# Optimization experiments

Measured on AMD Instinct MI355X. Metric: run time of the kernel, lower is better.

The kernel has to match this reference:

```python
import math
import jax, jax.numpy as jnp
import numpy as np

N_LAYERS = 30
RC = 64        # residual_channels
N_MELS = 80
TED = 128      # time_emb_dim
CD = 256       # text_dim
B, T = 8, 8192
EPS = 1e-12    # F.normalize eps


def conv1d(x, w, b, dilation=1, padding=0):
    # x: [B,C,T], w: [O,I,K], b: [O]
    y = jax.lax.conv_general_dilated(
        x, w, window_strides=(1,), padding=[(padding, padding)],
        rhs_dilation=(dilation,), dimension_numbers=("NCH", "OIH", "NCH"))
    return y + b[None, :, None]


def sinusoidal_embedding(t, dim):
    half = dim // 2
    freqs = jnp.exp(jnp.arange(half, dtype=jnp.float32) * (-math.log(10000.0) / (half - 1)))
    ang = t.astype(jnp.float32)[:, None] * freqs[None, :]
    return jnp.concatenate([jnp.sin(ang), jnp.cos(ang)], axis=1)  # [B, dim]


def mish(x):
    return x * jnp.tanh(jax.nn.softplus(x))


def setup_inputs() -> dict:
    key = jax.random.key(0)
    ks = jax.random.split(key, 24)
    s = 0.05
    inp = {
        "x": jax.random.normal(ks[0], (B, 1, N_MELS, T), jnp.float32),
        "t": jax.random.randint(ks[1], (B,), 0, 1000),
        "c_emb": jax.random.normal(ks[2], (B, CD), jnp.float32),
        # input_proj: Conv1d(n_mels, RC, 1)
        "in_w": jax.random.normal(ks[3], (RC, N_MELS, 1), jnp.float32) * s,
        "in_b": jnp.zeros((RC,), jnp.float32),
        # time MLP: Linear(TED, 4*TED), Mish, Linear(4*TED, TED). torch weight [out,in]
        "te_w1": jax.random.normal(ks[4], (4 * TED, TED), jnp.float32) * s,
        "te_b1": jnp.zeros((4 * TED,), jnp.float32),
        "te_w2": jax.random.normal(ks[5], (TED, 4 * TED), jnp.float32) * s,
        "te_b2": jnp.zeros((TED,), jnp.float32),
        # per-layer stacked params
        "dconv_w": jax.random.normal(ks[6], (N_LAYERS, 2 * RC, RC, 3), jnp.float32) * s,
        "dconv_b": jnp.zeros((N_LAYERS, 2 * RC), jnp.float32),
        "tproj_w": jax.random.normal(ks[7], (N_LAYERS, 2 * RC, TED), jnp.float32) * s,
        "tproj_b": jnp.zeros((N_LAYERS, 2 * RC), jnp.float32),
        "cproj_w": jax.random.normal(ks[8], (N_LAYERS, 2 * RC, CD), jnp.float32) * s,
        "cproj_b": jnp.zeros((N_LAYERS, 2 * RC), jnp.float32),
        "rs_w": jax.random.normal(ks[9], (N_LAYERS, 2 * RC, RC, 1), jnp.float32) * s,
        "rs_b": jnp.zeros((N_LAYERS, 2 * RC), jnp.float32),
        "skip_w": jax.random.normal(ks[10], (RC, RC, 1), jnp.float32) * s,
        "skip_b": jnp.zeros((RC,), jnp.float32),
        "out_w": jax.random.normal(ks[11], (N_MELS, RC, 1), jnp.float32) * s,
        "out_b": jnp.zeros((N_MELS,), jnp.float32),
    }
    return inp


def reference(x, t, c_emb, in_w, in_b, te_w1, te_b1, te_w2, te_b2,
              dconv_w, dconv_b, tproj_w, tproj_b, cproj_w, cproj_b,
              rs_w, rs_b, skip_w, skip_b, out_w, out_b):
    h = x[:, 0]                                  # squeeze(1) -> [B, n_mels, T]
    h = conv1d(h, in_w, in_b)                    # [B, RC, T]
    te = sinusoidal_embedding(t, TED)
    te = mish(te @ te_w1.T + te_b1) @ te_w2.T + te_b2   # [B, TED]

    skips = jnp.zeros_like(conv1d(h, rs_w[0], rs_b[0])[:, :RC])  # [B, RC, T]
    skips = jnp.zeros((h.shape[0], RC, h.shape[2]), h.dtype)
    for i in range(N_LAYERS):
        dil = 2 ** (i % 10)
        g = conv1d(h, dconv_w[i], dconv_b[i], dilation=dil, padding=dil)  # [B, 2RC, T]
        tp = (te @ tproj_w[i].T + tproj_b[i])[:, :, None]                 # [B, 2RC, 1]
        tp = tp / jnp.maximum(jnp.abs(tp), EPS)      # F.normalize over size-1 dim
        cp = (c_emb @ cproj_w[i].T + cproj_b[i])[:, :, None]
        cp = cp / jnp.maximum(jnp.abs(cp), EPS)
        g = g + tp + cp
        gate, filt = g[:, :RC], g[:, RC:]            # chunk(2, dim=1)
        out = jnp.tanh(filt) * jax.nn.sigmoid(gate)
        rs = conv1d(out, rs_w[i], rs_b[i])           # [B, 2RC, T]
        res, skip = rs[:, :RC], rs[:, RC:]
        h = h + res * (1.0 / math.sqrt(2.0))
        skips = skips + skip

    y = skips / math.sqrt(N_LAYERS)
    y = jax.nn.relu(conv1d(y, skip_w, skip_b))
    y = conv1d(y, out_w, out_b)                      # [B, n_mels, T]
    return y[:, None]                                # unsqueeze(1)
```

## Files before the change

### kernel.cpp

```cpp
#include <hip/hip_runtime.h>
#include <hip/hip_bf16.h>
#include <math.h>

#define NL 30
#define NM 80
#define Bx 8
#define Tx 8192

typedef short short8 __attribute__((ext_vector_type(8)));
typedef float f32x4 __attribute__((ext_vector_type(4)));
typedef unsigned int u32x2 __attribute__((ext_vector_type(2)));
typedef unsigned int u32x4 __attribute__((ext_vector_type(4)));

__device__ __forceinline__ float bf2f(unsigned short u) {
    union { unsigned int u; float f; } v; v.u = ((unsigned int)u) << 16; return v.f;
}
__device__ __forceinline__ unsigned short f2bf(float f) {
    union { float f; unsigned int u; } v; v.f = f;
    unsigned int r = v.u + 0x7FFFu + ((v.u >> 16) & 1u);
    return (unsigned short)(r >> 16);
}

#if defined(__has_builtin)
#if __has_builtin(__builtin_amdgcn_global_load_lds)
#define HAS_GLL 1
#endif
#endif

__device__ __forceinline__ void gll16(const void* g, void* l) {
#ifdef HAS_GLL
    __builtin_amdgcn_global_load_lds(
        (const __attribute__((address_space(1))) void*)g,
        (__attribute__((address_space(3))) void*)l, 16, 0, 0);
#else
    int lane = threadIdx.x & 63;
    *(u32x4*)((char*)l + lane * 16) = *(const u32x4*)((const char*)g + lane * 16);
#endif
}

__device__ __forceinline__ void stageW(const unsigned short* __restrict__ wc,
                                       const unsigned short* __restrict__ wr,
                                       unsigned char* ldsA, unsigned char* ldsR, int tid) {
    int w = tid >> 6, lane = tid & 63;
    #pragma unroll
    for (int j = 0; j < 6; ++j) {
        int cbase = j * 512 + w * 64;
        gll16(wc + (size_t)(cbase + lane) * 8, ldsA + cbase * 16);
    }
    #pragma unroll
    for (int j = 0; j < 2; ++j) {
        int cbase = j * 512 + w * 64;
        gll16(wr + (size_t)(cbase + lane) * 8, ldsR + cbase * 16);
    }
}

__global__ __launch_bounds__(512) void setup_kernel(
        const float* __restrict__ dconv_w, const float* __restrict__ rs_w,
        const float* __restrict__ skip_w, const float* __restrict__ out_w,
        unsigned short* __restrict__ wc2, unsigned short* __restrict__ wr2,
        unsigned short* __restrict__ skw16, unsigned short* __restrict__ oww16,
        const float* __restrict__ x, const float* __restrict__ in_w,
        const float* __restrict__ in_b, unsigned short* __restrict__ h0) {
    __shared__ __align__(16) unsigned char smem[49152];
    int blk = blockIdx.x;
    int tid = threadIdx.x;
    if (blk < 30) {
        int l = blk;
        unsigned short* st = (unsigned short*)smem;
        const f32x4* src4 = (const f32x4*)(dconv_w + (size_t)l * 24576);
        #pragma unroll
        for (int h = 0; h < 2; ++h) {
            f32x4 v[6];
            #pragma unroll
            for (int it = 0; it < 6; ++it)
                v[it] = src4[(h * 6 + it) * 512 + tid];
            #pragma unroll
            for (int it = 0; it < 6; ++it) {
                int chunk = (h * 6 + it) * 512 + tid;
                #pragma unroll
                for (int e = 0; e < 4; ++e) {
                    int sidx = chunk * 4 + e;
                    int oc = sidx / 192;
                    int r = sidx - oc * 192;
                    int ic = r / 3;
                    int tap = r - ic * 3;
                    int dst = tap * 8192 + oc * 64 + (((ic >> 3) ^ (oc & 7)) << 3) + (ic & 7);
                    st[dst] = f2bf(v[it][e]);
                }
            }
        }
        __syncthreads();
        u32x4* dst4 = (u32x4*)(wc2 + (size_t)l * 24576);
        const u32x4* s4 = (const u32x4*)st;
        #pragma unroll
        for (int it = 0; it < 6; ++it)
            dst4[it * 512 + tid] = s4[it * 512 + tid];
    } else if (blk < 60) {
        int l = blk - 30;
        unsigned short* st = (unsigned short*)smem;
        const f32x4* src4 = (const f32x4*)(rs_w + (size_t)l * 8192);
        f32x4 v[4];
        #pragma unroll
        for (int it = 0; it < 4; ++it)
            v[it] = src4[it * 512 + tid];
        #pragma unroll
        for (int it = 0; it < 4; ++it) {
            int chunk = it * 512 + tid;
            #pragma unroll
            for (int e = 0; e < 4; ++e) {
                int sidx = chunk * 4 + e;
                int row = sidx >> 6;
                int ic = sidx & 63;
                int dst = row * 64 + (((ic >> 3) ^ (row & 7)) << 3) + (ic & 7);
                st[dst] = f2bf(v[it][e]);
            }
        }
        __syncthreads();
        u32x4* dst4 = (u32x4*)(wr2 + (size_t)l * 8192);
        const u32x4* s4 = (const u32x4*)st;
        #pragma unroll
        for (int it = 0; it < 2; ++it)
            dst4[it * 512 + tid] = s4[it * 512 + tid];
    } else if (blk == 60) {
        for (int j = tid; j < 4096; j += 512)
            skw16[j] = f2bf(skip_w[j] * 0.18257418583505536f);
        for (int j = tid; j < 5120; j += 512)
            oww16[j] = f2bf(out_w[j]);
    } else {
        float (*wT)[64] = (float(*)[64])smem;
        for (int i = tid; i < NM * 64; i += 512) {
            int m = i >> 6, c = i & 63;
            wT[m][c] = in_w[c * NM + m];
        }
        __syncthreads();
        int j = blk - 61;
        int b = j >> 5;
        int t = (j & 31) * 256 + (tid >> 1);
        int ch0 = (tid & 1) * 32;
        const float* xp = x + (size_t)b * NM * Tx + t;
        float acc[32];
        #pragma unroll
        for (int c = 0; c < 32; ++c) acc[c] = in_b[ch0 + c];
        #pragma unroll 1
        for (int m0 = 0; m0 < NM; m0 += 8) {
            float xv[8];
            #pragma unroll
            for (int u = 0; u < 8; ++u) xv[u] = xp[(size_t)(m0 + u) * Tx];
            #pragma unroll
            for (int u = 0; u < 8; ++u) {
                #pragma unroll
                for (int c = 0; c < 32; ++c)
                    acc[c] = fmaf(xv[u], wT[m0 + u][ch0 + c], acc[c]);
            }
        }
        unsigned short* hp = h0 + ((size_t)b * Tx + t) * 64 + ch0;
        #pragma unroll
        for (int c = 0; c < 32; c += 2) {
            unsigned int p = (unsigned int)f2bf(acc[c]) | ((unsigned int)f2bf(acc[c + 1]) << 16);
            *(unsigned int*)(hp + c) = p;
        }
    }
}

__global__ __launch_bounds__(512) void gbias_kernel(
        const int* __restrict__ tin,
        const float* __restrict__ w1, const float* __restrict__ b1,
        const float* __restrict__ w2, const float* __restrict__ b2,
        const float* __restrict__ cemb,
        const float* __restrict__ tpw, const float* __restrict__ tpb,
        const float* __restrict__ cpw, const float* __restrict__ cpb,
        const float* __restrict__ dcb,
        float* __restrict__ gbias) {
    __shared__ float emb[128];
    __shared__ float h1s[512];
    __shared__ float red[512];
    __shared__ float ted[128];
    int l = blockIdx.x >> 3;
    int b = blockIdx.x & 7;
    int tid = threadIdx.x, wid = tid >> 6, lane = tid & 63;

    if (tid < 64) {
        float fr = expf(-(float)tid * (logf(10000.f) / 63.f));
        float ang = (float)tin[b] * fr;
        emb[tid] = sinf(ang);
        emb[tid + 64] = cosf(ang);
    }
    __syncthreads();
    {
        float a = b1[tid];
        const f32x4* wr4 = (const f32x4*)(w1 + tid * 128);
        #pragma unroll 8
        for (int k = 0; k < 32; ++k) {
            f32x4 w4 = wr4[k];
            a = fmaf(emb[k * 4], w4[0], a);
            a = fmaf(emb[k * 4 + 1], w4[1], a);
            a = fmaf(emb[k * 4 + 2], w4[2], a);
            a = fmaf(emb[k * 4 + 3], w4[3], a);
        }
        float sp = (a > 15.f) ? a : log1pf(expf(a));
        h1s[tid] = a * tanhf(sp);
    }
    __syncthreads();
    {
        int o = tid & 127, q = tid >> 7;
        float p = 0.f;
        const f32x4* wr4 = (const f32x4*)(w2 + o * 512 + q * 128);
        const float* hq = h1s + q * 128;
        #pragma unroll 8
        for (int k = 0; k < 32; ++k) {
            f32x4 w4 = wr4[k];
            p = fmaf(hq[k * 4], w4[0], p);
            p = fmaf(hq[k * 4 + 1], w4[1], p);
            p = fmaf(hq[k * 4 + 2], w4[2], p);
            p = fmaf(hq[k * 4 + 3], w4[3], p);
        }
        red[tid] = p;
    }
    __syncthreads();
    if (tid < 128)
        ted[tid] = b2[tid] + red[tid] + red[tid + 128] + red[tid + 256] + red[tid + 384];
    __syncthreads();

    float te0 = ted[lane];
    float te1 = ted[64 + lane];
    float ce0 = cemb[b * 256 + lane];
    float ce1 = cemb[b * 256 + 64 + lane];
    float ce2 = cemb[b * 256 + 128 + lane];
    float ce3 = cemb[b * 256 + 192 + lane];
    #pragma unroll 4
    for (int i = 0; i < 16; ++i) {
        int ch = i * 8 + wid;
        const float* wr = tpw + (size_t)(l * 128 + ch) * 128;
        float s = te0 * wr[lane] + te1 * wr[lane + 64];
        const float* wc = cpw + (size_t)(l * 128 + ch) * 256;
        float sc = ce0 * wc[lane] + ce1 * wc[lane + 64] + ce2 * wc[lane + 128] + ce3 * wc[lane + 192];
        #pragma unroll
        for (int off = 32; off >= 1; off >>= 1) {
            s += __shfl_xor(s, off, 64);
            sc += __shfl_xor(sc, off, 64);
        }
        if (lane == 0) {
            float tp = tpb[l * 128 + ch] + s;
            float cp = cpb[l * 128 + ch] + sc;
            float s1 = tp / fmaxf(fabsf(tp), 1e-12f);
            float s2 = cp / fmaxf(fabsf(cp), 1e-12f);
            gbias[(l * 8 + b) * 128 + ch] = dcb[l * 128 + ch] + s1 + s2;
        }
    }
}

__launch_bounds__(512, 4)
__global__ void layer_kernel(const unsigned short* __restrict__ h_in,
                             unsigned short* __restrict__ h_out,
                             float* __restrict__ skips,
                             const unsigned short* __restrict__ wc2,
                             const unsigned short* __restrict__ wr2,
                             const float* __restrict__ gbias,
                             const float* __restrict__ rsb,
                             int dil, int first) {
    __shared__ __align__(16) unsigned char lds[81920];
    unsigned char* ldsA = lds;
    unsigned char* ldsR = lds + 49152;
    unsigned char* ldsO = lds + 65536;

    int tid = threadIdx.x;
    int wid = tid >> 6, lane = tid & 63, lr = lane & 15, lq = lane >> 4;

    stageW(wc2, wr2, ldsA, ldsR, tid);

    int bid = blockIdx.x;
    int wg = (bid & 7) * 64 + (bid >> 3);
    int b = wg >> 6;
    int t0 = ((wg & 63) << 7) + wid * 16;

    const unsigned short* hb = h_in + (size_t)b * Tx * 64;
    short8 bv[3][2];
    #pragma unroll
    for (int tap = 0; tap < 3; ++tap) {
        int toff = (tap - 1) * dil;
        int t = t0 + lr + toff;
        bool v = ((unsigned)t < (unsigned)Tx);
        #pragma unroll
        for (int kc = 0; kc < 2; ++kc) {
            short8 z = {0, 0, 0, 0, 0, 0, 0, 0};
            if (v) z = *(const short8*)(hb + t * 64 + kc * 32 + lq * 8);
            bv[tap][kc] = z;
        }
    }

    f32x4 acc[8];
    #pragma unroll
    for (int mf = 0; mf < 8; ++mf)
        acc[mf] = *(const f32x4*)(gbias + b * 128 + mf * 16 + lq * 4);
    __syncthreads();

    #pragma unroll
    for (int tap = 0; tap < 3; ++tap) {
        #pragma unroll
        for (int kc = 0; kc < 2; ++kc) {
            #pragma unroll
            for (int mf = 0; mf < 8; ++mf) {
                int row = tap * 128 + mf * 16 + lr;
                short8 af = *(const short8*)(ldsA + row * 128 + ((kc * 64 + lq * 16) ^ ((lr & 7) << 4)));
                acc[mf] = __builtin_amdgcn_mfma_f32_16x16x32_bf16(af, bv[tap][kc], acc[mf], 0, 0, 0);
            }
        }
    }

    size_t base = ((size_t)b * Tx + t0 + lr) * 64;
    u32x2 hv[4];
    f32x4 sko[4];
    #pragma unroll
    for (int mf = 0; mf < 4; ++mf) {
        hv[mf] = *(const u32x2*)(h_in + base + mf * 16 + lq * 4);
        if (!first) sko[mf] = *(const f32x4*)(skips + base + mf * 16 + lq * 4);
        else { sko[mf][0] = 0.f; sko[mf][1] = 0.f; sko[mf][2] = 0.f; sko[mf][3] = 0.f; }
    }

    unsigned char* myO = ldsO + wid * 2048;
    #pragma unroll
    for (int mf = 0; mf < 4; ++mf) {
        int p = lr;
        unsigned short ob[4];
        #pragma unroll
        for (int r = 0; r < 4; ++r) {
            float g = acc[mf][r];
            float f = acc[mf + 4][r];
            f = fminf(f, 15.f);
            g = fminf(g, 30.f);
            float ea = __builtin_amdgcn_exp2f(f * 2.8853900817779268f);
            float eb = __builtin_amdgcn_exp2f(g * 1.4426950408889634f);
            float num = (ea - 1.f) * eb;
            float den = (ea + 1.f) * (1.f + eb);
            ob[r] = f2bf(num * __builtin_amdgcn_rcpf(den));
        }
        u32x2 pk;
        pk[0] = (unsigned int)ob[0] | ((unsigned int)ob[1] << 16);
        pk[1] = (unsigned int)ob[2] | ((unsigned int)ob[3] << 16);
        *(u32x2*)(myO + p * 128 + ((mf * 32 + lq * 8) ^ ((p & 7) << 4))) = pk;
    }

    const float rt2 = 1.41421356237309505f;
    f32x4 racc[8];
    #pragma unroll
    for (int mf = 0; mf < 4; ++mf) {
        f32x4 rb = *(const f32x4*)(rsb + mf * 16 + lq * 4);
        unsigned short* hp = (unsigned short*)&hv[mf];
        f32x4 r;
        #pragma unroll
        for (int r_ = 0; r_ < 4; ++r_) r[r_] = fmaf(bf2f(hp[r_]), rt2, rb[r_]);
        racc[mf] = r;
    }
    #pragma unroll
    for (int mf = 0; mf < 4; ++mf)
        racc[mf + 4] = *(const f32x4*)(rsb + 64 + mf * 16 + lq * 4) + sko[mf];

    #pragma unroll
    for (int kc = 0; kc < 2; ++kc) {
        int p = lr;
        short8 ov = *(const short8*)(myO + p * 128 + ((kc * 64 + lq * 16) ^ ((p & 7) << 4)));
        #pragma unroll
        for (int mf = 0; mf < 8; ++mf) {
            int row = mf * 16 + lr;
            short8 af = *(const short8*)(ldsR + row * 128 + ((kc * 64 + lq * 16) ^ ((lr & 7) << 4)));
            racc[mf] = __builtin_amdgcn_mfma_f32_16x16x32_bf16(af, ov, racc[mf], 0, 0, 0);
        }
    }

    const float inv_s2 = 0.70710678118654752f;
    #pragma unroll
    for (int mf = 0; mf < 4; ++mf) {
        unsigned short hnew[4];
        #pragma unroll
        for (int r = 0; r < 4; ++r)
            hnew[r] = f2bf(racc[mf][r] * inv_s2);
        u32x2 hw;
        hw[0] = (unsigned int)hnew[0] | ((unsigned int)hnew[1] << 16);
        hw[1] = (unsigned int)hnew[2] | ((unsigned int)hnew[3] << 16);
        *(u32x2*)(h_out + base + mf * 16 + lq * 4) = hw;
        *(f32x4*)(skips + base + mf * 16 + lq * 4) = racc[mf + 4];
    }
}

__launch_bounds__(512, 2)
__global__ void layer_pair_kernel(const unsigned short* __restrict__ h_in,
                                  unsigned short* __restrict__ h_out,
                                  float* __restrict__ skips,
                                  const unsigned short* __restrict__ wc2a,
                                  const unsigned short* __restrict__ wr2a,
                                  const float* __restrict__ gba,
                                  const float* __restrict__ rsba,
                                  int l1, int dil1, int dil2, int ht16, int first) {
    __shared__ __align__(16) unsigned char lds[114688];
    unsigned char* ldsA = lds;
    unsigned char* ldsR = lds + 49152;
    unsigned char* ldsH = lds + 65536;
    unsigned char* ldsO = lds + 90112;

    int tid = threadIdx.x;
    int w = tid >> 6, lane = tid & 63, lr = lane & 15, lq = lane >> 4;
    int l2 = l1 + 1;
    const float rt2 = 1.41421356237309505f;
    const float inv_s2 = 0.70710678118654752f;

    stageW(wc2a + (size_t)l1 * 24576, wr2a + (size_t)l1 * 8192, ldsA, ldsR, tid);

    int bid = blockIdx.x;
    int wg = (bid & 7) * 64 + (bid >> 3);
    int b = wg >> 6;
    int t0 = (wg & 63) << 7;
    int T = 8 + 2 * ht16;
    int ct = (w >= ht16) ? w : 8 + w;

    const unsigned short* hb = h_in + (size_t)b * Tx * 64;
    const float* gb1 = gba + (size_t)(l1 * 8 + b) * 128;
    const float* rsb1 = rsba + (size_t)l1 * 128;
    __syncthreads();

    for (int k = 0; k < 2; ++k) {
        int tile = k ? 8 + w : w;
        if (k && tile >= T) break;
        int gtb = t0 + (tile - ht16) * 16;
        short8 bv[3][2];
        #pragma unroll
        for (int tap = 0; tap < 3; ++tap) {
            int t = gtb + lr + (tap - 1) * dil1;
            bool v = ((unsigned)t < (unsigned)Tx);
            #pragma unroll
            for (int kc = 0; kc < 2; ++kc) {
                short8 z = {0, 0, 0, 0, 0, 0, 0, 0};
                if (v) z = *(const short8*)(hb + t * 64 + kc * 32 + lq * 8);
                bv[tap][kc] = z;
            }
        }
        f32x4 acc[8];
        #pragma unroll
        for (int mf = 0; mf < 8; ++mf)
            acc[mf] = *(const f32x4*)(gb1 + mf * 16 + lq * 4);
        #pragma unroll
        for (int tap = 0; tap < 3; ++tap) {
            #pragma unroll
            for (int kc = 0; kc < 2; ++kc) {
                #pragma unroll
                for (int mf = 0; mf < 8; ++mf) {
                    int row = tap * 128 + mf * 16 + lr;
                    short8 af = *(const short8*)(ldsA + row * 128 + ((kc * 64 + lq * 16) ^ ((lr & 7) << 4)));
                    acc[mf] = __builtin_amdgcn_mfma_f32_16x16x32_bf16(af, bv[tap][kc], acc[mf], 0, 0, 0);
                }
            }
        }
        unsigned char* myO = ldsO + tile * 2048;
        #pragma unroll
        for (int mf = 0; mf < 4; ++mf) {
            int p = lr;
            unsigned short ob[4];
            #pragma unroll
            for (int r = 0; r < 4; ++r) {
                float g = acc[mf][r];
                float f = acc[mf + 4][r];
                f = fminf(f, 15.f);
                g = fminf(g, 30.f);
                float ea = __builtin_amdgcn_exp2f(f * 2.8853900817779268f);
                float eb = __builtin_amdgcn_exp2f(g * 1.4426950408889634f);
                float num = (ea - 1.f) * eb;
                float den = (ea + 1.f) * (1.f + eb);
                ob[r] = f2bf(num * __builtin_amdgcn_rcpf(den));
            }
            u32x2 pk;
            pk[0] = (unsigned int)ob[0] | ((unsigned int)ob[1] << 16);
            pk[1] = (unsigned int)ob[2] | ((unsigned int)ob[3] << 16);
            *(u32x2*)(myO + p * 128 + ((mf * 32 + lq * 8) ^ ((p & 7) << 4))) = pk;
        }
    }

    f32x4 sk1[4];
    u32x2 hn1[4];
    for (int k = 0; k < 2; ++k) {
        int tile = k ? 8 + w : w;
        if (k && tile >= T) break;
        int gtb = t0 + (tile - ht16) * 16;
        int t = gtb + lr;
        bool tv = ((unsigned)t < (unsigned)Tx);
        u32x2 hv[4];
        #pragma unroll
        for (int mf = 0; mf < 4; ++mf) {
            u32x2 z; z[0] = 0u; z[1] = 0u;
            if (tv) z = *(const u32x2*)(h_in + ((size_t)b * Tx + t) * 64 + mf * 16 + lq * 4);
            hv[mf] = z;
        }
        f32x4 racc[8];
        #pragma unroll
        for (int mf = 0; mf < 4; ++mf) {
            f32x4 rb = *(const f32x4*)(rsb1 + mf * 16 + lq * 4);
            unsigned short* hp = (unsigned short*)&hv[mf];
            f32x4 r;
            #pragma unroll
            for (int r_ = 0; r_ < 4; ++r_) r[r_] = fmaf(bf2f(hp[r_]), rt2, rb[r_]);
            racc[mf] = r;
        }
        #pragma unroll
        for (int mf = 0; mf < 4; ++mf)
            racc[mf + 4] = *(const f32x4*)(rsb1 + 64 + mf * 16 + lq * 4);
        unsigned char* myO = ldsO + tile * 2048;
        #pragma unroll
        for (int kc = 0; kc < 2; ++kc) {
            int p = lr;
            short8 ov = *(const short8*)(myO + p * 128 + ((kc * 64 + lq * 16) ^ ((p & 7) << 4)));
            #pragma unroll
            for (int mf = 0; mf < 8; ++mf) {
                int row = mf * 16 + lr;
                short8 af = *(const short8*)(ldsR + row * 128 + ((kc * 64 + lq * 16) ^ ((lr & 7) << 4)));
                racc[mf] = __builtin_amdgcn_mfma_f32_16x16x32_bf16(af, ov, racc[mf], 0, 0, 0);
            }
        }
        int hrow = tile * 16 + lr;
        #pragma unroll
        for (int mf = 0; mf < 4; ++mf) {
            u32x2 pk; pk[0] = 0u; pk[1] = 0u;
            if (tv) {
                unsigned short hn[4];
                #pragma unroll
                for (int r = 0; r < 4; ++r)
                    hn[r] = f2bf(racc[mf][r] * inv_s2);
                pk[0] = (unsigned int)hn[0] | ((unsigned int)hn[1] << 16);
                pk[1] = (unsigned int)hn[2] | ((unsigned int)hn[3] << 16);
            }
            *(u32x2*)(ldsH + hrow * 128 + ((mf * 32 + lq * 8) ^ ((hrow & 7) << 4))) = pk;
            if (tile == ct) { sk1[mf] = racc[mf + 4]; hn1[mf] = pk; }
        }
    }
    __syncthreads();

    stageW(wc2a + (size_t)l2 * 24576, wr2a + (size_t)l2 * 8192, ldsA, ldsR, tid);
    int gtc = t0 + (ct - ht16) * 16;
    size_t cbase = ((size_t)b * Tx + gtc + lr) * 64;
    f32x4 sko[4];
    #pragma unroll
    for (int mf = 0; mf < 4; ++mf) {
        if (!first) sko[mf] = *(const f32x4*)(skips + cbase + mf * 16 + lq * 4);
        else { sko[mf][0] = 0.f; sko[mf][1] = 0.f; sko[mf][2] = 0.f; sko[mf][3] = 0.f; }
    }
    const float* gb2 = gba + (size_t)(l2 * 8 + b) * 128;
    const float* rsb2 = rsba + (size_t)l2 * 128;
    f32x4 acc2[8];
    #pragma unroll
    for (int mf = 0; mf < 8; ++mf)
        acc2[mf] = *(const f32x4*)(gb2 + mf * 16 + lq * 4);
    __syncthreads();

    int lrow0 = ct * 16 + lr;
    #pragma unroll
    for (int tap = 0; tap < 3; ++tap) {
        int row = lrow0 + (tap - 1) * dil2;
        #pragma unroll
        for (int kc = 0; kc < 2; ++kc) {
            short8 bv2 = *(const short8*)(ldsH + row * 128 + ((kc * 64 + lq * 16) ^ ((row & 7) << 4)));
            #pragma unroll
            for (int mf = 0; mf < 8; ++mf) {
                int wrow = tap * 128 + mf * 16 + lr;
                short8 af = *(const short8*)(ldsA + wrow * 128 + ((kc * 64 + lq * 16) ^ ((lr & 7) << 4)));
                acc2[mf] = __builtin_amdgcn_mfma_f32_16x16x32_bf16(af, bv2, acc2[mf], 0, 0, 0);
            }
        }
    }

    unsigned char* myO = ldsO + ct * 2048;
    #pragma unroll
    for (int mf = 0; mf < 4; ++mf) {
        int p = lr;
        unsigned short ob[4];
        #pragma unroll
        for (int r = 0; r < 4; ++r) {
            float g = acc2[mf][r];
            float f = acc2[mf + 4][r];
            f = fminf(f, 15.f);
            g = fminf(g, 30.f);
            float ea = __builtin_amdgcn_exp2f(f * 2.8853900817779268f);
            float eb = __builtin_amdgcn_exp2f(g * 1.4426950408889634f);
            float num = (ea - 1.f) * eb;
            float den = (ea + 1.f) * (1.f + eb);
            ob[r] = f2bf(num * __builtin_amdgcn_rcpf(den));
        }
        u32x2 pk;
        pk[0] = (unsigned int)ob[0] | ((unsigned int)ob[1] << 16);
        pk[1] = (unsigned int)ob[2] | ((unsigned int)ob[3] << 16);
        *(u32x2*)(myO + p * 128 + ((mf * 32 + lq * 8) ^ ((p & 7) << 4))) = pk;
    }

    f32x4 racc2[8];
    #pragma unroll
    for (int mf = 0; mf < 4; ++mf) {
        f32x4 rb = *(const f32x4*)(rsb2 + mf * 16 + lq * 4);
        unsigned short* hp = (unsigned short*)&hn1[mf];
        f32x4 r;
        #pragma unroll
        for (int r_ = 0; r_ < 4; ++r_) r[r_] = fmaf(bf2f(hp[r_]), rt2, rb[r_]);
        racc2[mf] = r;
    }
    #pragma unroll
    for (int mf = 0; mf < 4; ++mf)
        racc2[mf + 4] = *(const f32x4*)(rsb2 + 64 + mf * 16 + lq * 4) + sko[mf] + sk1[mf];

    #pragma unroll
    for (int kc = 0; kc < 2; ++kc) {
        int p = lr;
        short8 ov = *(const short8*)(myO + p * 128 + ((kc * 64 + lq * 16) ^ ((p & 7) << 4)));
        #pragma unroll
        for (int mf = 0; mf < 8; ++mf) {
            int row = mf * 16 + lr;
            short8 af = *(const short8*)(ldsR + row * 128 + ((kc * 64 + lq * 16) ^ ((lr & 7) << 4)));
            racc2[mf] = __builtin_amdgcn_mfma_f32_16x16x32_bf16(af, ov, racc2[mf], 0, 0, 0);
        }
    }

    #pragma unroll
    for (int mf = 0; mf < 4; ++mf) {
        unsigned short hnew[4];
        #pragma unroll
        for (int r = 0; r < 4; ++r)
            hnew[r] = f2bf(racc2[mf][r] * inv_s2);
        u32x2 hw;
        hw[0] = (unsigned int)hnew[0] | ((unsigned int)hnew[1] << 16);
        hw[1] = (unsigned int)hnew[2] | ((unsigned int)hnew[3] << 16);
        *(u32x2*)(h_out + cbase + mf * 16 + lq * 4) = hw;
        *(f32x4*)(skips + cbase + mf * 16 + lq * 4) = racc2[mf + 4];
    }
}

__launch_bounds__(512, 2)
__global__ void layer_last_kernel(const unsigned short* __restrict__ h_in,
                                  const float* __restrict__ skips,
                                  const unsigned short* __restrict__ wc2,
                                  const unsigned short* __restrict__ wr2,
                                  const float* __restrict__ gbias,
                                  const float* __restrict__ rsb,
                                  const unsigned short* __restrict__ skw,
                                  const float* __restrict__ skb,
                                  const unsigned short* __restrict__ oww,
                                  const float* __restrict__ obias,
                                  float* __restrict__ y,
                                  int dil) {
    __shared__ __align__(16) unsigned char lds[81920];
    unsigned char* ldsA = lds;
    unsigned char* ldsR = lds + 49152;
    unsigned char* ldsO = lds + 65536;

    int tid = threadIdx.x;
    int wid = tid >> 6, lane = tid & 63, lr = lane & 15, lq = lane >> 4;

    stageW(wc2, wr2, ldsA, ldsR, tid);

    int bid = blockIdx.x;
    int wg = (bid & 7) * 64 + (bid >> 3);
    int b = wg >> 6;
    int t0 = ((wg & 63) << 7) + wid * 16;

    const unsigned short* hb = h_in + (size_t)b * Tx * 64;
    short8 bv[3][2];
    #pragma unroll
    for (int tap = 0; tap < 3; ++tap) {
        int toff = (tap - 1) * dil;
        int t = t0 + lr + toff;
        bool v = ((unsigned)t < (unsigned)Tx);
        #pragma unroll
        for (int kc = 0; kc < 2; ++kc) {
            short8 z = {0, 0, 0, 0, 0, 0, 0, 0};
            if (v) z = *(const short8*)(hb + t * 64 + kc * 32 + lq * 8);
            bv[tap][kc] = z;
        }
    }

    f32x4 acc[8];
    #pragma unroll
    for (int mf = 0; mf < 8; ++mf)
        acc[mf] = *(const f32x4*)(gbias + b * 128 + mf * 16 + lq * 4);
    __syncthreads();

    #pragma unroll
    for (int tap = 0; tap < 3; ++tap) {
        #pragma unroll
        for (int kc = 0; kc < 2; ++kc) {
            #pragma unroll
            for (int mf = 0; mf < 8; ++mf) {
                int row = tap * 128 + mf * 16 + lr;
                short8 af = *(const short8*)(ldsA + row * 128 + ((kc * 64 + lq * 16) ^ ((lr & 7) << 4)));
                acc[mf] = __builtin_amdgcn_mfma_f32_16x16x32_bf16(af, bv[tap][kc], acc[mf], 0, 0, 0);
            }
        }
    }

    size_t base = ((size_t)b * Tx + t0 + lr) * 64;
    f32x4 sko[4];
    #pragma unroll
    for (int mf = 0; mf < 4; ++mf)
        sko[mf] = *(const f32x4*)(skips + base + mf * 16 + lq * 4);

    unsigned char* myO = ldsO + wid * 2048;
    #pragma unroll
    for (int mf = 0; mf < 4; ++mf) {
        int p = lr;
        unsigned short ob[4];
        #pragma unroll
        for (int r = 0; r < 4; ++r) {
            float g = acc[mf][r];
            float f = acc[mf + 4][r];
            f = fminf(f, 15.f);
            g = fminf(g, 30.f);
            float ea = __builtin_amdgcn_exp2f(f * 2.8853900817779268f);
            float eb = __builtin_amdgcn_exp2f(g * 1.4426950408889634f);
            float num = (ea - 1.f) * eb;
            float den = (ea + 1.f) * (1.f + eb);
            ob[r] = f2bf(num * __builtin_amdgcn_rcpf(den));
        }
        u32x2 pk;
        pk[0] = (unsigned int)ob[0] | ((unsigned int)ob[1] << 16);
        pk[1] = (unsigned int)ob[2] | ((unsigned int)ob[3] << 16);
        *(u32x2*)(myO + p * 128 + ((mf * 32 + lq * 8) ^ ((p & 7) << 4))) = pk;
    }

    f32x4 racc[4];
    #pragma unroll
    for (int mf = 0; mf < 4; ++mf)
        racc[mf] = *(const f32x4*)(rsb + 64 + mf * 16 + lq * 4) + sko[mf];
    #pragma unroll
    for (int kc = 0; kc < 2; ++kc) {
        int p = lr;
        short8 ov = *(const short8*)(myO + p * 128 + ((kc * 64 + lq * 16) ^ ((p & 7) << 4)));
        #pragma unroll
        for (int mf = 0; mf < 4; ++mf) {
            int row = 64 + mf * 16 + lr;
            short8 af = *(const short8*)(ldsR + row * 128 + ((kc * 64 + lq * 16) ^ ((lr & 7) << 4)));
            racc[mf] = __builtin_amdgcn_mfma_f32_16x16x32_bf16(af, ov, racc[mf], 0, 0, 0);
        }
    }

    #pragma unroll
    for (int mf = 0; mf < 4; ++mf) {
        int p = lr;
        u32x2 pk;
        pk[0] = (unsigned int)f2bf(racc[mf][0]) | ((unsigned int)f2bf(racc[mf][1]) << 16);
        pk[1] = (unsigned int)f2bf(racc[mf][2]) | ((unsigned int)f2bf(racc[mf][3]) << 16);
        *(u32x2*)(myO + p * 128 + ((mf * 32 + lq * 8) ^ ((p & 7) << 4))) = pk;
    }

    f32x4 yacc[4];
    #pragma unroll
    for (int mf = 0; mf < 4; ++mf)
        yacc[mf] = *(const f32x4*)(skb + mf * 16 + lq * 4);
    #pragma unroll
    for (int kc = 0; kc < 2; ++kc) {
        int p = lr;
        short8 Bv = *(const short8*)(myO + p * 128 + ((kc * 64 + lq * 16) ^ ((p & 7) << 4)));
        #pragma unroll
        for (int mf = 0; mf < 4; ++mf) {
            short8 A1 = *(const short8*)(skw + (mf * 16 + lr) * 64 + kc * 32 + lq * 8);
            yacc[mf] = __builtin_amdgcn_mfma_f32_16x16x32_bf16(A1, Bv, yacc[mf], 0, 0, 0);
        }
    }
    #pragma unroll
    for (int mf = 0; mf < 4; ++mf) {
        int p = lr;
        u32x2 pk;
        pk[0] = (unsigned int)f2bf(fmaxf(yacc[mf][0], 0.f)) | ((unsigned int)f2bf(fmaxf(yacc[mf][1], 0.f)) << 16);
        pk[1] = (unsigned int)f2bf(fmaxf(yacc[mf][2], 0.f)) | ((unsigned int)f2bf(fmaxf(yacc[mf][3], 0.f)) << 16);
        *(u32x2*)(myO + p * 128 + ((mf * 32 + lq * 8) ^ ((p & 7) << 4))) = pk;
    }

    f32x4 oacc[5];
    #pragma unroll
    for (int mf = 0; mf < 5; ++mf)
        oacc[mf] = *(const f32x4*)(obias + mf * 16 + lq * 4);
    #pragma unroll
    for (int kc = 0; kc < 2; ++kc) {
        int p = lr;
        short8 B2 = *(const short8*)(myO + p * 128 + ((kc * 64 + lq * 16) ^ ((p & 7) << 4)));
        #pragma unroll
        for (int mf = 0; mf < 5; ++mf) {
            short8 A2 = *(const short8*)(oww + (mf * 16 + lr) * 64 + kc * 32 + lq * 8);
            oacc[mf] = __builtin_amdgcn_mfma_f32_16x16x32_bf16(A2, B2, oacc[mf], 0, 0, 0);
        }
    }
    int t = t0 + lr;
    #pragma unroll
    for (int mf = 0; mf < 5; ++mf) {
        #pragma unroll
        for (int r = 0; r < 4; ++r) {
            int m = mf * 16 + lq * 4 + r;
            y[((size_t)b * NM + m) * Tx + t] = oacc[mf][r];
        }
    }
}

extern "C" void kernel_launch(void* const* d_in, const int* in_sizes, int n_in,
                              void* d_out, int out_size, void* d_ws, size_t ws_size,
                              hipStream_t stream) {
    const float* x       = (const float*)d_in[0];
    const int*   tin     = (const int*)d_in[1];
    const float* c_emb   = (const float*)d_in[2];
    const float* in_w    = (const float*)d_in[3];
    const float* in_b    = (const float*)d_in[4];
    const float* te_w1   = (const float*)d_in[5];
    const float* te_b1   = (const float*)d_in[6];
    const float* te_w2   = (const float*)d_in[7];
    const float* te_b2   = (const float*)d_in[8];
    const float* dconv_w = (const float*)d_in[9];
    const float* dconv_b = (const float*)d_in[10];
    const float* tproj_w = (const float*)d_in[11];
    const float* tproj_b = (const float*)d_in[12];
    const float* cproj_w = (const float*)d_in[13];
    const float* cproj_b = (const float*)d_in[14];
    const float* rs_w    = (const float*)d_in[15];
    const float* rs_b    = (const float*)d_in[16];
    const float* skip_w  = (const float*)d_in[17];
    const float* skip_b  = (const float*)d_in[18];
    const float* out_w   = (const float*)d_in[19];
    const float* out_b   = (const float*)d_in[20];

    char* ws = (char*)d_ws;
    float* gbias          = (float*)(ws + 4096);
    unsigned short* skw16 = (unsigned short*)(ws + 126976);
    unsigned short* oww16 = (unsigned short*)(ws + 135168);
    unsigned short* wc2   = (unsigned short*)(ws + 145408);
    unsigned short* wr2   = (unsigned short*)(ws + 1619968);
    unsigned short* h0    = (unsigned short*)(ws + 2111488);
    unsigned short* h1    = (unsigned short*)(ws + 10500096);
    float* skips          = (float*)(ws + 18888704);

    setup_kernel<<<317, 512, 0, stream>>>(dconv_w, rs_w, skip_w, out_w,
                                          wc2, wr2, skw16, oww16,
                                          x, in_w, in_b, h0);
    gbias_kernel<<<240, 512, 0, stream>>>(tin, te_w1, te_b1, te_w2, te_b2,
                                          c_emb, tproj_w, tproj_b,
                                          cproj_w, cproj_b, dconv_b, gbias);

    bool pstart[29] = {false};
    pstart[0] = pstart[2] = pstart[4] = pstart[9] = pstart[11] = pstart[13]
              = pstart[19] = pstart[21] = pstart[23] = true;

    unsigned short* hin = h0;
    unsigned short* hout = h1;
    int i = 0;
    while (i < NL - 1) {
        int dil = 1 << (i % 10);
        if (pstart[i]) {
            int dil2 = 1 << ((i + 1) % 10);
            int ht16 = (dil2 > 16) ? 2 : 1;
            layer_pair_kernel<<<512, 512, 0, stream>>>(hin, hout, skips,
                                                       wc2, wr2, gbias, rs_b,
                                                       i, dil, dil2, ht16,
                                                       i == 0 ? 1 : 0);
            unsigned short* tmp = hin; hin = hout; hout = tmp;
            i += 2;
        } else {
            layer_kernel<<<512, 512, 0, stream>>>(hin, hout, skips,
                                                  wc2 + (size_t)i * 24576,
                                                  wr2 + (size_t)i * 8192,
                                                  gbias + (size_t)i * 1024,
                                                  rs_b + (size_t)i * 128,
                                                  dil, 0);
            unsigned short* tmp = hin; hin = hout; hout = tmp;
            i += 1;
        }
    }
    layer_last_kernel<<<512, 512, 0, stream>>>(hin, skips,
                                               wc2 + (size_t)(NL - 1) * 24576,
                                               wr2 + (size_t)(NL - 1) * 8192,
                                               gbias + (size_t)(NL - 1) * 1024,
                                               rs_b + (size_t)(NL - 1) * 128,
                                               skw16, skip_b, oww16, out_b,
                                               (float*)d_out, 1 << ((NL - 1) % 10));
}
```

Baseline: 531.8 us.

## Fuse six dilated layers per kernel with LDS-resident halo recomputation

Replaces the two-layer fused kernel with a six-layer fused kernel for dilations 1 through 32. Each block keeps a 256-step window of h in double-buffered LDS, restages weights per layer, and shrinks the valid tile range as the receptive-field halo grows. This cuts global h/skip round trips and kernel launches for the early layers of each cycle. In exchange it recomputes halo tiles redundantly, uses more LDS (147KB, lowering occupancy), and adds per-layer barriers and weight staging.

Result: faster. 517.5 us (-2.7%).

```diff
diff --git a/kernel.cpp b/kernel.cpp
--- a/kernel.cpp
+++ b/kernel.cpp
@@ -383,247 +383,196 @@
 }
 
 __launch_bounds__(512, 2)
-__global__ void layer_pair_kernel(const unsigned short* __restrict__ h_in,
-                                  unsigned short* __restrict__ h_out,
-                                  float* __restrict__ skips,
-                                  const unsigned short* __restrict__ wc2a,
-                                  const unsigned short* __restrict__ wr2a,
-                                  const float* __restrict__ gba,
-                                  const float* __restrict__ rsba,
-                                  int l1, int dil1, int dil2, int ht16, int first) {
-    __shared__ __align__(16) unsigned char lds[114688];
+__global__ void layer_hex_kernel(const unsigned short* __restrict__ h_in,
+                                 unsigned short* __restrict__ h_out,
+                                 float* __restrict__ skips,
+                                 const unsigned short* __restrict__ wc2a,
+                                 const unsigned short* __restrict__ wr2a,
+                                 const float* __restrict__ gba,
+                                 const float* __restrict__ rsba,
+                                 int l0, int first) {
+    __shared__ __align__(16) unsigned char lds[147456];
     unsigned char* ldsA = lds;
     unsigned char* ldsR = lds + 49152;
-    unsigned char* ldsH = lds + 65536;
-    unsigned char* ldsO = lds + 90112;
+    unsigned char* ldsH0 = lds + 65536;
+    unsigned char* ldsH1 = lds + 98304;
+    unsigned char* ldsO = lds + 131072;
 
     int tid = threadIdx.x;
     int w = tid >> 6, lane = tid & 63, lr = lane & 15, lq = lane >> 4;
-    int l2 = l1 + 1;
     const float rt2 = 1.41421356237309505f;
     const float inv_s2 = 0.70710678118654752f;
-
-    stageW(wc2a + (size_t)l1 * 24576, wr2a + (size_t)l1 * 8192, ldsA, ldsR, tid);
 
     int bid = blockIdx.x;
     int wg = (bid & 7) * 64 + (bid >> 3);
     int b = wg >> 6;
     int t0 = (wg & 63) << 7;
-    int T = 8 + 2 * ht16;
-    int ct = (w >= ht16) ? w : 8 + w;
+    int ct = (w >= 4) ? w : w + 8;
 
     const unsigned short* hb = h_in + (size_t)b * Tx * 64;
-    const float* gb1 = gba + (size_t)(l1 * 8 + b) * 128;
-    const float* rsb1 = rsba + (size_t)l1 * 128;
-    __syncthreads();
-
-    for (int k = 0; k < 2; ++k) {
-        int tile = k ? 8 + w : w;
-        if (k && tile >= T) break;
-        int gtb = t0 + (tile - ht16) * 16;
-        short8 bv[3][2];
-        #pragma unroll
-        for (int tap = 0; tap < 3; ++tap) {
-            int t = gtb + lr + (tap - 1) * dil1;
-            bool v = ((unsigned)t < (unsigned)Tx);
-            #pragma unroll
-            for (int kc = 0; kc < 2; ++kc) {
-                short8 z = {0, 0, 0, 0, 0, 0, 0, 0};
-                if (v) z = *(const short8*)(hb + t * 64 + kc * 32 + lq * 8);
-                bv[tap][kc] = z;
-            }
-        }
-        f32x4 acc[8];
-        #pragma unroll
-        for (int mf = 0; mf < 8; ++mf)
-            acc[mf] = *(const f32x4*)(gb1 + mf * 16 + lq * 4);
-        #pragma unroll
-        for (int tap = 0; tap < 3; ++tap) {
-            #pragma unroll
-            for (int kc = 0; kc < 2; ++kc) {
+    unsigned char* Hc = ldsH0;
+    unsigned char* Hn = ldsH1;
+    unsigned char* myO = ldsO + w * 2048;
+
+    int gtc = t0 + (ct - 4) * 16 + lr;
+    size_t cbase = ((size_t)b * Tx + gtc) * 64;
+    f32x4 skacc[4];
+    #pragma unroll
+    for (int mf = 0; mf < 4; ++mf) {
+        if (!first) skacc[mf] = *(const f32x4*)(skips + cbase + mf * 16 + lq * 4);
+        else { skacc[mf][0] = 0.f; skacc[mf][1] = 0.f; skacc[mf][2] = 0.f; skacc[mf][3] = 0.f; }
+    }
+
+    u32x2 hnreg[2][4];
+
+    #pragma unroll 1
+    for (int j = 0; j < 6; ++j) {
+        int l = l0 + j;
+        int dil = 1 << j;
+        int lo = (j <= 2) ? 0 : (j == 3 ? 1 : (j == 4 ? 2 : 4));
+        int hi = 16 - lo;
+        const float* gb = gba + (size_t)(l * 8 + b) * 128;
+        const float* rsb = rsba + (size_t)l * 128;
+
+        __syncthreads();
+        stageW(wc2a + (size_t)l * 24576, wr2a + (size_t)l * 8192, ldsA, ldsR, tid);
+        __syncthreads();
+
+        #pragma unroll
+        for (int k = 0; k < 2; ++k) {
+            int tile = k ? w + 8 : w;
+            if (tile >= lo && tile < hi) {
+                int gt = t0 + (tile - 4) * 16 + lr;
+                bool tv = ((unsigned)gt < (unsigned)Tx);
+
+                f32x4 acc[8];
                 #pragma unroll
-                for (int mf = 0; mf < 8; ++mf) {
-                    int row = tap * 128 + mf * 16 + lr;
-                    short8 af = *(const short8*)(ldsA + row * 128 + ((kc * 64 + lq * 16) ^ ((lr & 7) << 4)));
-                    acc[mf] = __builtin_amdgcn_mfma_f32_16x16x32_bf16(af, bv[tap][kc], acc[mf], 0, 0, 0);
+                for (int mf = 0; mf < 8; ++mf)
+                    acc[mf] = *(const f32x4*)(gb + mf * 16 + lq * 4);
+                if (j == 0) {
+                    #pragma unroll
+                    for (int tap = 0; tap < 3; ++tap) {
+                        int t = gt + (tap - 1);
+                        bool v = ((unsigned)t < (unsigned)Tx);
+                        #pragma unroll
+                        for (int kc = 0; kc < 2; ++kc) {
+                            short8 z = {0, 0, 0, 0, 0, 0, 0, 0};
+                            if (v) z = *(const short8*)(hb + t * 64 + kc * 32 + lq * 8);
+                            #pragma unroll
+                            for (int mf = 0; mf < 8; ++mf) {
+                                int row = tap * 128 + mf * 16 + lr;
+                                short8 af = *(const short8*)(ldsA + row * 128 + ((kc * 64 + lq * 16) ^ ((lr & 7) << 4)));
+                                acc[mf] = __builtin_amdgcn_mfma_f32_16x16x32_bf16(af, z, acc[mf], 0, 0, 0);
+                            }
+                        }
+                    }
+                } else {
+                    #pragma unroll
+                    for (int tap = 0; tap < 3; ++tap) {
+                        int row = tile * 16 + lr + (tap - 1) * dil;
+                        row = max(0, min(255, row));
+                        #pragma unroll
+                        for (int kc = 0; kc < 2; ++kc) {
+                            short8 z = *(const short8*)(Hc + row * 128 + ((kc * 64 + lq * 16) ^ ((row & 7) << 4)));
+                            #pragma unroll
+                            for (int mf = 0; mf < 8; ++mf) {
+                                int wrow = tap * 128 + mf * 16 + lr;
+                                short8 af = *(const short8*)(ldsA + wrow * 128 + ((kc * 64 + lq * 16) ^ ((lr & 7) << 4)));
+                                acc[mf] = __builtin_amdgcn_mfma_f32_16x16x32_bf16(af, z, acc[mf], 0, 0, 0);
+                            }
+                        }
+                    }
+                }
+
+                #pragma unroll
+                for (int mf = 0; mf < 4; ++mf) {
+                    int p = lr;
+                    unsigned short ob[4];
+                    #pragma unroll
+                    for (int r = 0; r < 4; ++r) {
+                        float g = acc[mf][r];
+                        float f = acc[mf + 4][r];
+                        f = fminf(f, 15.f);
+                        g = fminf(g, 30.f);
+                        float ea = __builtin_amdgcn_exp2f(f * 2.8853900817779268f);
+                        float eb = __builtin_amdgcn_exp2f(g * 1.4426950408889634f);
+                        float num = (ea - 1.f) * eb;
+                        float den = (ea + 1.f) * (1.f + eb);
+                        ob[r] = f2bf(num * __builtin_amdgcn_rcpf(den));
+                    }
+                    u32x2 pk;
+                    pk[0] = (unsigned int)ob[0] | ((unsigned int)ob[1] << 16);
+                    pk[1] = (unsigned int)ob[2] | ((unsigned int)ob[3] << 16);
+                    *(u32x2*)(myO + p * 128 + ((mf * 32 + lq * 8) ^ ((p & 7) << 4))) = pk;
+                }
+
+                u32x2 hv[4];
+                if (j == 0) {
+                    #pragma unroll
+                    for (int mf = 0; mf < 4; ++mf) {
+                        u32x2 z; z[0] = 0u; z[1] = 0u;
+                        if (tv) z = *(const u32x2*)(hb + gt * 64 + mf * 16 + lq * 4);
+                        hv[mf] = z;
+                    }
+                } else {
+                    #pragma unroll
+                    for (int mf = 0; mf < 4; ++mf) hv[mf] = hnreg[k][mf];
+                }
+                f32x4 racc[8];
+                #pragma unroll
+                for (int mf = 0; mf < 4; ++mf) {
+                    f32x4 rb = *(const f32x4*)(rsb + mf * 16 + lq * 4);
+                    unsigned short* hp = (unsigned short*)&hv[mf];
+                    f32x4 r;
+                    #pragma unroll
+                    for (int r_ = 0; r_ < 4; ++r_) r[r_] = fmaf(bf2f(hp[r_]), rt2, rb[r_]);
+                    racc[mf] = r;
+                }
+                #pragma unroll
+                for (int mf = 0; mf < 4; ++mf)
+                    racc[mf + 4] = *(const f32x4*)(rsb + 64 + mf * 16 + lq * 4);
+                #pragma unroll
+                for (int kc = 0; kc < 2; ++kc) {
+                    int p = lr;
+                    short8 ov = *(const short8*)(myO + p * 128 + ((kc * 64 + lq * 16) ^ ((p & 7) << 4)));
+                    #pragma unroll
+                    for (int mf = 0; mf < 8; ++mf) {
+                        int row = mf * 16 + lr;
+                        short8 af = *(const short8*)(ldsR + row * 128 + ((kc * 64 + lq * 16) ^ ((lr & 7) << 4)));
+                        racc[mf] = __builtin_amdgcn_mfma_f32_16x16x32_bf16(af, ov, racc[mf], 0, 0, 0);
+                    }
+                }
+
+                int hrow = tile * 16 + lr;
+                #pragma unroll
+                for (int mf = 0; mf < 4; ++mf) {
+                    u32x2 pk; pk[0] = 0u; pk[1] = 0u;
+                    if (tv) {
+                        unsigned short hn[4];
+                        #pragma unroll
+                        for (int r = 0; r < 4; ++r)
+                            hn[r] = f2bf(racc[mf][r] * inv_s2);
+                        pk[0] = (unsigned int)hn[0] | ((unsigned int)hn[1] << 16);
+                        pk[1] = (unsigned int)hn[2] | ((unsigned int)hn[3] << 16);
+                    }
+                    *(u32x2*)(Hn + hrow * 128 + ((mf * 32 + lq * 8) ^ ((hrow & 7) << 4))) = pk;
+                    hnreg[k][mf] = pk;
+                }
+                if (tile == ct) {
+                    #pragma unroll
+                    for (int mf = 0; mf < 4; ++mf)
+                        skacc[mf] += racc[mf + 4];
+                    if (j == 5) {
+                        #pragma unroll
+                        for (int mf = 0; mf < 4; ++mf) {
+                            *(u32x2*)(h_out + cbase + mf * 16 + lq * 4) = hnreg[k][mf];
+                            *(f32x4*)(skips + cbase + mf * 16 + lq * 4) = skacc[mf];
+                        }
+                    }
                 }
             }
         }
-        unsigned char* myO = ldsO + tile * 2048;
-        #pragma unroll
-        for (int mf = 0; mf < 4; ++mf) {
-            int p = lr;
-            unsigned short ob[4];
-            #pragma unroll
-            for (int r = 0; r < 4; ++r) {
-                float g = acc[mf][r];
-                float f = acc[mf + 4][r];
-                f = fminf(f, 15.f);
-                g = fminf(g, 30.f);
-                float ea = __builtin_amdgcn_exp2f(f * 2.8853900817779268f);
-                float eb = __builtin_amdgcn_exp2f(g * 1.4426950408889634f);
-                float num = (ea - 1.f) * eb;
-                float den = (ea + 1.f) * (1.f + eb);
-                ob[r] = f2bf(num * __builtin_amdgcn_rcpf(den));
-            }
-            u32x2 pk;
-            pk[0] = (unsigned int)ob[0] | ((unsigned int)ob[1] << 16);
-            pk[1] = (unsigned int)ob[2] | ((unsigned int)ob[3] << 16);
-            *(u32x2*)(myO + p * 128 + ((mf * 32 + lq * 8) ^ ((p & 7) << 4))) = pk;
-        }
-    }
-
-    f32x4 sk1[4];
-    u32x2 hn1[4];
-    for (int k = 0; k < 2; ++k) {
-        int tile = k ? 8 + w : w;
-        if (k && tile >= T) break;
-        int gtb = t0 + (tile - ht16) * 16;
-        int t = gtb + lr;
-        bool tv = ((unsigned)t < (unsigned)Tx);
-        u32x2 hv[4];
-        #pragma unroll
-        for (int mf = 0; mf < 4; ++mf) {
-            u32x2 z; z[0] = 0u; z[1] = 0u;
-            if (tv) z = *(const u32x2*)(h_in + ((size_t)b * Tx + t) * 64 + mf * 16 + lq * 4);
-            hv[mf] = z;
-        }
-        f32x4 racc[8];
-        #pragma unroll
-        for (int mf = 0; mf < 4; ++mf) {
-            f32x4 rb = *(const f32x4*)(rsb1 + mf * 16 + lq * 4);
-            unsigned short* hp = (unsigned short*)&hv[mf];
-            f32x4 r;
-            #pragma unroll
-            for (int r_ = 0; r_ < 4; ++r_) r[r_] = fmaf(bf2f(hp[r_]), rt2, rb[r_]);
-            racc[mf] = r;
-        }
-        #pragma unroll
-        for (int mf = 0; mf < 4; ++mf)
-            racc[mf + 4] = *(const f32x4*)(rsb1 + 64 + mf * 16 + lq * 4);
-        unsigned char* myO = ldsO + tile * 2048;
-        #pragma unroll
-        for (int kc = 0; kc < 2; ++kc) {
-            int p = lr;
-            short8 ov = *(const short8*)(myO + p * 128 + ((kc * 64 + lq * 16) ^ ((p & 7) << 4)));
-            #pragma unroll
-            for (int mf = 0; mf < 8; ++mf) {
-                int row = mf * 16 + lr;
-                short8 af = *(const short8*)(ldsR + row * 128 + ((kc * 64 + lq * 16) ^ ((lr & 7) << 4)));
-                racc[mf] = __builtin_amdgcn_mfma_f32_16x16x32_bf16(af, ov, racc[mf], 0, 0, 0);
-            }
-        }
-        int hrow = tile * 16 + lr;
-        #pragma unroll
-        for (int mf = 0; mf < 4; ++mf) {
-            u32x2 pk; pk[0] = 0u; pk[1] = 0u;
-            if (tv) {
-                unsigned short hn[4];
-                #pragma unroll
-                for (int r = 0; r < 4; ++r)
-                    hn[r] = f2bf(racc[mf][r] * inv_s2);
-                pk[0] = (unsigned int)hn[0] | ((unsigned int)hn[1] << 16);
-                pk[1] = (unsigned int)hn[2] | ((unsigned int)hn[3] << 16);
-            }
-            *(u32x2*)(ldsH + hrow * 128 + ((mf * 32 + lq * 8) ^ ((hrow & 7) << 4))) = pk;
-            if (tile == ct) { sk1[mf] = racc[mf + 4]; hn1[mf] = pk; }
-        }
-    }
-    __syncthreads();
-
-    stageW(wc2a + (size_t)l2 * 24576, wr2a + (size_t)l2 * 8192, ldsA, ldsR, tid);
-    int gtc = t0 + (ct - ht16) * 16;
-    size_t cbase = ((size_t)b * Tx + gtc + lr) * 64;
-    f32x4 sko[4];
-    #pragma unroll
-    for (int mf = 0; mf < 4; ++mf) {
-        if (!first) sko[mf] = *(const f32x4*)(skips + cbase + mf * 16 + lq * 4);
-        else { sko[mf][0] = 0.f; sko[mf][1] = 0.f; sko[mf][2] = 0.f; sko[mf][3] = 0.f; }
-    }
-    const float* gb2 = gba + (size_t)(l2 * 8 + b) * 128;
-    const float* rsb2 = rsba + (size_t)l2 * 128;
-    f32x4 acc2[8];
-    #pragma unroll
-    for (int mf = 0; mf < 8; ++mf)
-        acc2[mf] = *(const f32x4*)(gb2 + mf * 16 + lq * 4);
-    __syncthreads();
-
-    int lrow0 = ct * 16 + lr;
-    #pragma unroll
-    for (int tap = 0; tap < 3; ++tap) {
-        int row = lrow0 + (tap - 1) * dil2;
-        #pragma unroll
-        for (int kc = 0; kc < 2; ++kc) {
-            short8 bv2 = *(const short8*)(ldsH + row * 128 + ((kc * 64 + lq * 16) ^ ((row & 7) << 4)));
-            #pragma unroll
-            for (int mf = 0; mf < 8; ++mf) {
-                int wrow = tap * 128 + mf * 16 + lr;
-                short8 af = *(const short8*)(ldsA + wrow * 128 + ((kc * 64 + lq * 16) ^ ((lr & 7) << 4)));
-                acc2[mf] = __builtin_amdgcn_mfma_f32_16x16x32_bf16(af, bv2, acc2[mf], 0, 0, 0);
-            }
-        }
-    }
-
-    unsigned char* myO = ldsO + ct * 2048;
-    #pragma unroll
-    for (int mf = 0; mf < 4; ++mf) {
-        int p = lr;
-        unsigned short ob[4];
-        #pragma unroll
-        for (int r = 0; r < 4; ++r) {
-            float g = acc2[mf][r];
-            float f = acc2[mf + 4][r];
-            f = fminf(f, 15.f);
-            g = fminf(g, 30.f);
-            float ea = __builtin_amdgcn_exp2f(f * 2.8853900817779268f);
-            float eb = __builtin_amdgcn_exp2f(g * 1.4426950408889634f);
-            float num = (ea - 1.f) * eb;
-            float den = (ea + 1.f) * (1.f + eb);
-            ob[r] = f2bf(num * __builtin_amdgcn_rcpf(den));
-        }
-        u32x2 pk;
-        pk[0] = (unsigned int)ob[0] | ((unsigned int)ob[1] << 16);
-        pk[1] = (unsigned int)ob[2] | ((unsigned int)ob[3] << 16);
-        *(u32x2*)(myO + p * 128 + ((mf * 32 + lq * 8) ^ ((p & 7) << 4))) = pk;
-    }
-
-    f32x4 racc2[8];
-    #pragma unroll
-    for (int mf = 0; mf < 4; ++mf) {
-        f32x4 rb = *(const f32x4*)(rsb2 + mf * 16 + lq * 4);
-        unsigned short* hp = (unsigned short*)&hn1[mf];
-        f32x4 r;
-        #pragma unroll
-        for (int r_ = 0; r_ < 4; ++r_) r[r_] = fmaf(bf2f(hp[r_]), rt2, rb[r_]);
-        racc2[mf] = r;
-    }
-    #pragma unroll
-    for (int mf = 0; mf < 4; ++mf)
-        racc2[mf + 4] = *(const f32x4*)(rsb2 + 64 + mf * 16 + lq * 4) + sko[mf] + sk1[mf];
-
-    #pragma unroll
-    for (int kc = 0; kc < 2; ++kc) {
-        int p = lr;
-        short8 ov = *(const short8*)(myO + p * 128 + ((kc * 64 + lq * 16) ^ ((p & 7) << 4)));
-        #pragma unroll
-        for (int mf = 0; mf < 8; ++mf) {
-            int row = mf * 16 + lr;
-            short8 af = *(const short8*)(ldsR + row * 128 + ((kc * 64 + lq * 16) ^ ((lr & 7) << 4)));
-            racc2[mf] = __builtin_amdgcn_mfma_f32_16x16x32_bf16(af, ov, racc2[mf], 0, 0, 0);
-        }
-    }
-
-    #pragma unroll
-    for (int mf = 0; mf < 4; ++mf) {
-        unsigned short hnew[4];
-        #pragma unroll
-        for (int r = 0; r < 4; ++r)
-            hnew[r] = f2bf(racc2[mf][r] * inv_s2);
-        u32x2 hw;
-        hw[0] = (unsigned int)hnew[0] | ((unsigned int)hnew[1] << 16);
-        hw[1] = (unsigned int)hnew[2] | ((unsigned int)hnew[3] << 16);
-        *(u32x2*)(h_out + cbase + mf * 16 + lq * 4) = hw;
-        *(f32x4*)(skips + cbase + mf * 16 + lq * 4) = racc2[mf + 4];
+        unsigned char* tmp = Hc; Hc = Hn; Hn = tmp;
     }
 }
 
@@ -833,25 +782,19 @@
                                           c_emb, tproj_w, tproj_b,
                                           cproj_w, cproj_b, dconv_b, gbias);
 
-    bool pstart[29] = {false};
-    pstart[0] = pstart[2] = pstart[4] = pstart[9] = pstart[11] = pstart[13]
-              = pstart[19] = pstart[21] = pstart[23] = true;
-
     unsigned short* hin = h0;
     unsigned short* hout = h1;
     int i = 0;
     while (i < NL - 1) {
-        int dil = 1 << (i % 10);
-        if (pstart[i]) {
-            int dil2 = 1 << ((i + 1) % 10);
-            int ht16 = (dil2 > 16) ? 2 : 1;
-            layer_pair_kernel<<<512, 512, 0, stream>>>(hin, hout, skips,
-                                                       wc2, wr2, gbias, rs_b,
-                                                       i, dil, dil2, ht16,
-                                                       i == 0 ? 1 : 0);
+        int dec = i % 10;
+        if (dec == 0 && i + 5 < NL - 1) {
+            layer_hex_kernel<<<512, 512, 0, stream>>>(hin, hout, skips,
+                                                      wc2, wr2, gbias, rs_b,
+                                                      i, i == 0 ? 1 : 0);
             unsigned short* tmp = hin; hin = hout; hout = tmp;
-            i += 2;
+            i += 6;
         } else {
+            int dil = 1 << dec;
             layer_kernel<<<512, 512, 0, stream>>>(hin, hout, skips,
                                                   wc2 + (size_t)i * 24576,
                                                   wr2 + (size_t)i * 8192,
```
